# Optimization experiments

Hardware: AMD Instinct MI355X
Metric: run time of the kernel (lower is better)

## Reference

```python
import jax, jax.numpy as jnp
import numpy as np

EPS = 1e-6
GAIN = 0.3

def setup_inputs() -> dict:
    key = jax.random.key(0)
    k1, k2 = jax.random.split(key)
    B, C, H, W = 8, 1024, 64, 64
    C_MID = 8
    z = jax.random.normal(k1, (B, C, H, W), dtype=jnp.float32)
    # down conv weight (c_mid, c_in); up weight is its transpose (PCA-ish projector)
    W_down = jax.random.normal(k2, (C_MID, C), dtype=jnp.float32) / np.sqrt(C)
    return {"z": z, "W_down": W_down}

def reference(z, W_down):
    # GroupNorm(1, C, affine=False): normalize over (C,H,W) per sample
    mu = jnp.mean(z, axis=(1, 2, 3), keepdims=True)
    var = jnp.var(z, axis=(1, 2, 3), keepdims=True)
    x = (z - mu) * jax.lax.rsqrt(var + EPS)
    # 1x1 conv down: (B,C,H,W) x (M,C) -> (B,M,H,W)
    y = jnp.einsum('bchw,mc->bmhw', x, W_down)
    # 1x1 conv up with weight = down^T: (B,M,H,W) x (M,C) -> (B,C,H,W)
    r = jnp.einsum('bmhw,mc->bchw', y, W_down)
    return z + GAIN * r
```

## Files before the change

### kernel.cpp

```cpp
#include <hip/hip_runtime.h>
#include <math.h>

#define B    8
#define C    1024
#define M    8
#define HW   4096
#define EPS  1e-6f
#define GAIN 0.3f

#define NT   4
#define NC   16
#define NP   (NT*NC)
#define HWT  (HW/NT)
#define CCH  (C/NC)
#define TPB  256

#define OFF_YZP   0
#define OFF_STATP (OFF_YZP + B*NC*M*HW)
#define OFF_Y     (OFF_STATP + B*NP*2)

__global__ __launch_bounds__(TPB) void k1_partial(const float* __restrict__ z,
                                                  const float* __restrict__ Wd,
                                                  float* __restrict__ ws) {
    int bid = blockIdx.x;
    int nc  = bid % NC;
    int t   = (bid / NC) % NT;
    int b   = bid / (NC * NT);
    int tid = threadIdx.x;
    int hw  = t * HWT + tid * 4;
    int c0  = nc * CCH;

    float4 ym[M];
#pragma unroll
    for (int m = 0; m < M; ++m) ym[m] = make_float4(0.f, 0.f, 0.f, 0.f);
    float su = 0.f, sq = 0.f;

    const float* zp = z + ((size_t)(b * C + c0)) * HW + hw;
#pragma unroll 2
    for (int ci = 0; ci < CCH; ++ci) {
        float4 v = *reinterpret_cast<const float4*>(zp + (size_t)ci * HW);
        su += (v.x + v.y) + (v.z + v.w);
        sq += v.x * v.x + v.y * v.y + v.z * v.z + v.w * v.w;
        int c = c0 + ci;
#pragma unroll
        for (int m = 0; m < M; ++m) {
            float w = Wd[m * C + c];
            ym[m].x += w * v.x;
            ym[m].y += w * v.y;
            ym[m].z += w * v.z;
            ym[m].w += w * v.w;
        }
    }

    float* yzp = ws + OFF_YZP + ((size_t)(b * NC + nc) * M) * HW + hw;
#pragma unroll
    for (int m = 0; m < M; ++m)
        *reinterpret_cast<float4*>(yzp + (size_t)m * HW) = ym[m];

    __shared__ float red[2 * TPB];
    red[tid] = su;
    red[TPB + tid] = sq;
    __syncthreads();
    for (int s = TPB / 2; s > 0; s >>= 1) {
        if (tid < s) {
            red[tid] += red[tid + s];
            red[TPB + tid] += red[TPB + tid + s];
        }
        __syncthreads();
    }
    if (tid == 0) {
        float* st = ws + OFF_STATP + ((size_t)b * NP + t * NC + nc) * 2;
        st[0] = red[0];
        st[1] = red[TPB];
    }
}

__global__ __launch_bounds__(TPB) void k2_reduce_y(const float* __restrict__ Wd,
                                                   float* __restrict__ ws) {
    int bid   = blockIdx.x;
    int b     = bid >> 5;
    int m     = (bid & 31) >> 2;
    int hwblk = bid & 3;
    int tid   = threadIdx.x;
    int hw    = hwblk * 1024 + tid * 4;

    __shared__ float red[TPB];
    __shared__ float sh[3];

    {
        float sm = Wd[m * C + tid] + Wd[m * C + tid + 256] +
                   Wd[m * C + tid + 512] + Wd[m * C + tid + 768];
        red[tid] = sm;
        __syncthreads();
        for (int s = TPB / 2; s > 0; s >>= 1) {
            if (tid < s) red[tid] += red[tid + s];
            __syncthreads();
        }
        if (tid == 0) sh[0] = red[0];
    }
    if (tid < 64) {
        const float* sp = ws + OFF_STATP + ((size_t)b * NP + tid) * 2;
        float su = sp[0], sq = sp[1];
#pragma unroll
        for (int o = 32; o > 0; o >>= 1) {
            su += __shfl_down(su, o);
            sq += __shfl_down(sq, o);
        }
        if (tid == 0) {
            const float invN = 1.0f / (float)(C * HW);
            float mu  = su * invN;
            float var = sq * invN - mu * mu;
            sh[1] = mu;
            sh[2] = 1.0f / sqrtf(var + EPS);
        }
    }
    __syncthreads();
    float off  = sh[1] * sh[0];
    float istd = sh[2];

    float4 acc = make_float4(0.f, 0.f, 0.f, 0.f);
    const float* p = ws + OFF_YZP + ((size_t)b * NC * M + m) * HW + hw;
#pragma unroll
    for (int ncp = 0; ncp < NC; ++ncp) {
        float4 v = *reinterpret_cast<const float4*>(p + (size_t)ncp * M * HW);
        acc.x += v.x; acc.y += v.y; acc.z += v.z; acc.w += v.w;
    }
    float4 y;
    y.x = istd * (acc.x - off);
    y.y = istd * (acc.y - off);
    y.z = istd * (acc.z - off);
    y.w = istd * (acc.w - off);
    *reinterpret_cast<float4*>(ws + OFF_Y + ((size_t)b * M + m) * HW + hw) = y;
}

__global__ __launch_bounds__(TPB) void k3_apply(const float* __restrict__ z,
                                                const float* __restrict__ Wd,
                                                const float* __restrict__ ws,
                                                float* __restrict__ out) {
    int bid = blockIdx.x;
    int nc  = bid % NC;
    int t   = (bid / NC) % NT;
    int b   = bid / (NC * NT);
    int tid = threadIdx.x;
    int hw  = t * HWT + tid * 4;
    int c0  = nc * CCH;

    float4 y[M];
    const float* yp = ws + OFF_Y + (size_t)b * M * HW + hw;
#pragma unroll
    for (int m = 0; m < M; ++m)
        y[m] = *reinterpret_cast<const float4*>(yp + (size_t)m * HW);

    const float* zp = z + ((size_t)(b * C + c0)) * HW + hw;
    float* op = out + ((size_t)(b * C + c0)) * HW + hw;
#pragma unroll 4
    for (int ci = 0; ci < CCH; ++ci) {
        float4 v = *reinterpret_cast<const float4*>(zp + (size_t)ci * HW);
        int c = c0 + ci;
        float rx = 0.f, ry = 0.f, rz = 0.f, rw = 0.f;
#pragma unroll
        for (int m = 0; m < M; ++m) {
            float w = Wd[m * C + c];
            rx += w * y[m].x;
            ry += w * y[m].y;
            rz += w * y[m].z;
            rw += w * y[m].w;
        }
        float4 o;
        o.x = v.x + GAIN * rx;
        o.y = v.y + GAIN * ry;
        o.z = v.z + GAIN * rz;
        o.w = v.w + GAIN * rw;
        *reinterpret_cast<float4*>(op + (size_t)ci * HW) = o;
    }
}

extern "C" void kernel_launch(void* const* d_in, const int* in_sizes, int n_in,
                              void* d_out, int out_size, void* d_ws, size_t ws_size,
                              hipStream_t stream) {
    const float* z  = (const float*)d_in[0];
    const float* Wd = (const float*)d_in[1];
    float* out = (float*)d_out;
    float* ws  = (float*)d_ws;

    dim3 blk(TPB);
    k1_partial<<<dim3(B * NT * NC), blk, 0, stream>>>(z, Wd, ws);
    k2_reduce_y<<<dim3(B * M * 4), blk, 0, stream>>>(Wd, ws);
    k3_apply<<<dim3(B * NT * NC), blk, 0, stream>>>(z, Wd, ws, out);
}
```

Measured before the change: 81.68 us.

## Halve channel splits, use nontemporal output stores, warp-reduce stats in k2

Result: faster. 72.86 us (-10.8%).

```diff
diff --git a/kernel.cpp b/kernel.cpp
--- a/kernel.cpp
+++ b/kernel.cpp
@@ -9,11 +9,13 @@
 #define GAIN 0.3f
 
 #define NT   4
-#define NC   16
+#define NC   8
 #define NP   (NT*NC)
 #define HWT  (HW/NT)
 #define CCH  (C/NC)
 #define TPB  256
+
+typedef float floatx4 __attribute__((ext_vector_type(4)));
 
 #define OFF_YZP   0
 #define OFF_STATP (OFF_YZP + B*NC*M*HW)
@@ -36,7 +38,7 @@
     float su = 0.f, sq = 0.f;
 
     const float* zp = z + ((size_t)(b * C + c0)) * HW + hw;
-#pragma unroll 2
+#pragma unroll 4
     for (int ci = 0; ci < CCH; ++ci) {
         float4 v = *reinterpret_cast<const float4*>(zp + (size_t)ci * HW);
         su += (v.x + v.y) + (v.z + v.w);
@@ -82,41 +84,43 @@
     int m     = (bid & 31) >> 2;
     int hwblk = bid & 3;
     int tid   = threadIdx.x;
+    int wv    = tid >> 6;
+    int l     = tid & 63;
     int hw    = hwblk * 1024 + tid * 4;
 
-    __shared__ float red[TPB];
     __shared__ float sh[3];
 
-    {
-        float sm = Wd[m * C + tid] + Wd[m * C + tid + 256] +
-                   Wd[m * C + tid + 512] + Wd[m * C + tid + 768];
-        red[tid] = sm;
-        __syncthreads();
-        for (int s = TPB / 2; s > 0; s >>= 1) {
-            if (tid < s) red[tid] += red[tid + s];
-            __syncthreads();
+    if (wv == 0) {
+        float su = 0.f, sq = 0.f;
+        if (l < NP) {
+            const float* sp = ws + OFF_STATP + ((size_t)b * NP + l) * 2;
+            su = sp[0];
+            sq = sp[1];
         }
-        if (tid == 0) sh[0] = red[0];
-    }
-    if (tid < 64) {
-        const float* sp = ws + OFF_STATP + ((size_t)b * NP + tid) * 2;
-        float su = sp[0], sq = sp[1];
 #pragma unroll
-        for (int o = 32; o > 0; o >>= 1) {
+        for (int o = 16; o > 0; o >>= 1) {
             su += __shfl_down(su, o);
             sq += __shfl_down(sq, o);
         }
-        if (tid == 0) {
+        if (l == 0) {
             const float invN = 1.0f / (float)(C * HW);
             float mu  = su * invN;
             float var = sq * invN - mu * mu;
-            sh[1] = mu;
-            sh[2] = 1.0f / sqrtf(var + EPS);
+            sh[0] = mu;
+            sh[1] = 1.0f / sqrtf(var + EPS);
         }
+    } else if (wv == 1) {
+        float sm = 0.f;
+#pragma unroll
+        for (int k = 0; k < C / 64; ++k) sm += Wd[m * C + k * 64 + l];
+#pragma unroll
+        for (int o = 32; o > 0; o >>= 1) sm += __shfl_down(sm, o);
+        if (l == 0) sh[2] = sm;
     }
     __syncthreads();
-    float off  = sh[1] * sh[0];
-    float istd = sh[2];
+    float mu   = sh[0];
+    float istd = sh[1];
+    float off  = mu * sh[2];
 
     float4 acc = make_float4(0.f, 0.f, 0.f, 0.f);
     const float* p = ws + OFF_YZP + ((size_t)b * NC * M + m) * HW + hw;
@@ -166,12 +170,12 @@
             rz += w * y[m].z;
             rw += w * y[m].w;
         }
-        float4 o;
+        floatx4 o;
         o.x = v.x + GAIN * rx;
         o.y = v.y + GAIN * ry;
         o.z = v.z + GAIN * rz;
         o.w = v.w + GAIN * rw;
-        *reinterpret_cast<float4*>(op + (size_t)ci * HW) = o;
+        __builtin_nontemporal_store(o, reinterpret_cast<floatx4*>(op + (size_t)ci * HW));
     }
 }
 
```
